# Optimization experiments

Hardware: AMD Instinct MI355X
Metric: run time of the kernel (lower is better)

## Reference

```python
import jax, jax.numpy as jnp
import numpy as np

N_NODES = 100000
N_EDGES = 1600000
D_IN = 128
D_HID = 128
D_OUT = 10
N_GRAPHS = 512


def setup_inputs() -> dict:
    key = jax.random.key(0)
    ks = jax.random.split(key, 12)
    x = jax.random.normal(ks[0], (N_NODES, D_IN), dtype=jnp.float32)
    edge_index = jax.random.randint(ks[1], (2, N_EDGES), 0, N_NODES, dtype=jnp.int64)
    batch = jnp.sort(jax.random.randint(ks[2], (N_NODES,), 0, N_GRAPHS, dtype=jnp.int64))
    s = 1.0 / np.sqrt(D_HID)
    W0 = jax.random.normal(ks[3], (D_HID, D_IN), dtype=jnp.float32) * s
    b0 = jax.random.normal(ks[4], (D_HID,), dtype=jnp.float32) * s
    W1 = jax.random.normal(ks[5], (D_HID, D_HID), dtype=jnp.float32) * s
    b1 = jax.random.normal(ks[6], (D_HID,), dtype=jnp.float32) * s
    W2 = jax.random.normal(ks[7], (D_HID, D_HID), dtype=jnp.float32) * s
    b2 = jax.random.normal(ks[8], (D_HID,), dtype=jnp.float32) * s
    Wg = jax.random.normal(ks[9], (D_OUT, D_HID), dtype=jnp.float32) * s
    bg = jax.random.normal(ks[10], (D_OUT,), dtype=jnp.float32) * s
    return {"x": x, "edge_index": edge_index, "batch": batch,
            "W0": W0, "b0": b0, "W1": W1, "b1": b1, "W2": W2, "b2": b2,
            "Wg": Wg, "bg": bg}


def _gin_conv(x, src, dst, W, b):
    # GINConv with eps=0: Linear(x + sum_{j in N(i)} x_j)
    agg = jax.ops.segment_sum(x[src], dst, num_segments=N_NODES)  # [N, d]
    return (x + agg) @ W.T + b


def reference(x, edge_index, batch, W0, b0, W1, b1, W2, b2, Wg, bg):
    src, dst = edge_index[0], edge_index[1]
    h = jax.nn.relu(_gin_conv(x, src, dst, W0, b0))
    h = jax.nn.relu(_gin_conv(h, src, dst, W1, b1))
    h = _gin_conv(h, src, dst, W2, b2)
    # global_mean_pool over graph ids
    sums = jax.ops.segment_sum(h, batch, num_segments=N_GRAPHS)            # [G, d]
    counts = jax.ops.segment_sum(jnp.ones((N_NODES,), h.dtype), batch, num_segments=N_GRAPHS)
    pooled = sums / jnp.maximum(counts, 1.0)[:, None]                       # [G, d]
    return pooled @ Wg.T + bg                                               # [G, out]
```

## Files before the change

kernel.cpp:

```cpp
#include <hip/hip_runtime.h>

#define N_NODES 100000
#define N_EDGES 1600000
#define N_GRAPHS 512
#define NBUCK 391
#define EPB 8192
#define NB_SCAT ((N_EDGES + EPB - 1) / EPB)
#define CAPB 4864
#define CAP 5120

typedef _Float16 half8 __attribute__((ext_vector_type(8)));
typedef float floatx4 __attribute__((ext_vector_type(4)));

union U16 { uint4 u; half8 h; };

__global__ __launch_bounds__(256) void convert_f16(const float4* __restrict__ X4,
                                                   uint4* __restrict__ Xh) {
    int t = blockIdx.x * 256 + threadIdx.x;
    if (t >= N_NODES * 16) return;
    float4 a = X4[t * 2], b = X4[t * 2 + 1];
    U16 o;
    o.h[0] = (_Float16)a.x; o.h[1] = (_Float16)a.y;
    o.h[2] = (_Float16)a.z; o.h[3] = (_Float16)a.w;
    o.h[4] = (_Float16)b.x; o.h[5] = (_Float16)b.y;
    o.h[6] = (_Float16)b.z; o.h[7] = (_Float16)b.w;
    Xh[t] = o.u;
}

__global__ __launch_bounds__(256) void bucket_scatter(const int* __restrict__ src,
                                                      const int* __restrict__ dst,
                                                      int* __restrict__ gcur,
                                                      unsigned* __restrict__ pairs) {
    __shared__ int cnt[NBUCK];
    __shared__ int base[NBUCK];
    int tid = threadIdx.x;
    for (int i = tid; i < NBUCK; i += 256) cnt[i] = 0;
    __syncthreads();
    int e0 = blockIdx.x * EPB, e1 = min(e0 + EPB, N_EDGES);
    for (int e = e0 + tid; e < e1; e += 256) atomicAdd(&cnt[dst[e] >> 8], 1);
    __syncthreads();
    for (int i = tid; i < NBUCK; i += 256) {
        int v = cnt[i];
        base[i] = i * CAPB + (v ? atomicAdd(&gcur[i], v) : 0);
        cnt[i] = 0;
    }
    __syncthreads();
    for (int e = e0 + tid; e < e1; e += 256) {
        int d = dst[e], b = d >> 8;
        int r = atomicAdd(&cnt[b], 1);
        pairs[base[b] + r] = (unsigned)src[e] | ((unsigned)(d & 255) << 17);
    }
}

__global__ __launch_bounds__(64) void pack_w(const float* __restrict__ W0,
                                             const float* __restrict__ W1,
                                             const float* __restrict__ W2,
                                             uint4* __restrict__ Bp) {
    int b = blockIdx.x;
    int layer = b >> 5;
    int r = b & 31;
    int c = r >> 3, f = r & 7;
    const float* W = (layer == 0) ? W0 : (layer == 1) ? W1 : W2;
    int l = threadIdx.x;
    int col = f * 16 + (l & 15);
    int k0 = c * 32 + (l >> 4) * 8;
    U16 o;
    #pragma unroll
    for (int j = 0; j < 8; ++j) o.h[j] = (_Float16)W[col * 128 + k0 + j];
    Bp[layer * 2048 + (c * 8 + f) * 64 + l] = o.u;
}

__global__ __launch_bounds__(512) void bucket_scan(const int* __restrict__ gcur,
                                                   int* __restrict__ boff,
                                                   int* __restrict__ off) {
    __shared__ int ws[8];
    int tid = threadIdx.x;
    int v = (tid < NBUCK) ? gcur[tid] : 0;
    int lane = tid & 63, w = tid >> 6;
    int incl = v;
    #pragma unroll
    for (int s = 1; s < 64; s <<= 1) { int y = __shfl_up(incl, s, 64); if (lane >= s) incl += y; }
    if (lane == 63) ws[w] = incl;
    __syncthreads();
    if (tid < 8) {
        int t = ws[tid];
        #pragma unroll
        for (int s = 1; s < 8; s <<= 1) { int y = __shfl_up(t, s, 64); if (tid >= s) t += y; }
        ws[tid] = t;
    }
    __syncthreads();
    int excl = (w ? ws[w - 1] : 0) + incl - v;
    if (tid < NBUCK) boff[tid] = excl;
    if (tid == NBUCK - 1) boff[NBUCK] = excl + v;
    if (tid == 0) off[N_NODES] = N_EDGES;
}

__global__ __launch_bounds__(256) void bucket_fine(const unsigned* __restrict__ pairs,
                                                   const int* __restrict__ boff,
                                                   int* __restrict__ off,
                                                   int* __restrict__ srclist) {
    __shared__ int ncnt[256];
    __shared__ int ws[4];
    __shared__ int stage[CAP];
    int tid = threadIdx.x, b = blockIdx.x;
    int eLo = boff[b], m = boff[b + 1] - eLo;
    int sb = b * CAPB;
    ncnt[tid] = 0;
    __syncthreads();
    for (int t = tid; t < m; t += 256) {
        unsigned p = pairs[sb + t];
        atomicAdd(&ncnt[(p >> 17) & 255], 1);
    }
    __syncthreads();
    int v = ncnt[tid];
    int lane = tid & 63, w = tid >> 6;
    int incl = v;
    #pragma unroll
    for (int s = 1; s < 64; s <<= 1) { int y = __shfl_up(incl, s, 64); if (lane >= s) incl += y; }
    if (lane == 63) ws[w] = incl;
    __syncthreads();
    if (tid < 4) {
        int t = ws[tid];
        #pragma unroll
        for (int s = 1; s < 4; s <<= 1) { int y = __shfl_up(t, s, 64); if (tid >= s) t += y; }
        ws[tid] = t;
    }
    __syncthreads();
    int excl = (w ? ws[w - 1] : 0) + incl - v;
    int n = (b << 8) + tid;
    if (n < N_NODES) off[n] = eLo + excl;
    __syncthreads();
    ncnt[tid] = excl;
    __syncthreads();
    for (int t = tid; t < m; t += 256) {
        unsigned p = pairs[sb + t];
        int r = atomicAdd(&ncnt[(p >> 17) & 255], 1);
        int s = (int)(p & 0x1FFFFu);
        if (r < CAP) stage[r] = s;
        else srclist[eLo + r] = s;
    }
    __syncthreads();
    int lim = m < CAP ? m : CAP;
    for (int t = tid; t < lim; t += 256) srclist[eLo + t] = stage[t];
}

__global__ __launch_bounds__(256) void agg_f16(const uint4* __restrict__ Xh,
                                               uint4* __restrict__ Ah,
                                               const int* __restrict__ off,
                                               const int* __restrict__ srclist) {
    int t = blockIdx.x * 256 + threadIdx.x;
    int n = t >> 4, c = t & 15;
    if (n >= N_NODES) return;
    int j0 = off[n], j1 = off[n + 1];
    U16 acc; acc.u = Xh[(size_t)n * 16 + c];
    half8 a = acc.h;
    for (int j = j0; j < j1; j += 8) {
        int idx[8]; unsigned msk[8];
        #pragma unroll
        for (int i = 0; i < 8; ++i) {
            int jj = j + i;
            bool ok = jj < j1;
            int s = srclist[jj];
            idx[i] = ok ? s : n;
            msk[i] = ok ? 0xFFFFFFFFu : 0u;
        }
        U16 v[8];
        #pragma unroll
        for (int i = 0; i < 8; ++i) v[i].u = Xh[(size_t)idx[i] * 16 + c];
        #pragma unroll
        for (int i = 0; i < 8; ++i) {
            v[i].u.x &= msk[i]; v[i].u.y &= msk[i];
            v[i].u.z &= msk[i]; v[i].u.w &= msk[i];
            a += v[i].h;
        }
    }
    U16 o; o.h = a;
    Ah[(size_t)n * 16 + c] = o.u;
}

__global__ __launch_bounds__(256) void gemm_mfma(const _Float16* __restrict__ Ah,
                                                 const uint4* __restrict__ Bp,
                                                 const float* __restrict__ bias,
                                                 _Float16* __restrict__ H, int doRelu) {
    int tid = threadIdx.x;
    int wid = tid >> 6, lane = tid & 63;
    int nbase = blockIdx.x * 128 + wid * 32;
    int lrow = lane & 15;
    int lk = (lane >> 4) * 8;
    int row0 = min(nbase + lrow, N_NODES - 1);
    int row1 = min(nbase + 16 + lrow, N_NODES - 1);

    floatx4 acc[2][8];
    #pragma unroll
    for (int r = 0; r < 2; ++r)
        #pragma unroll
        for (int f = 0; f < 8; ++f) acc[r][f] = (floatx4)0.f;

    #pragma unroll
    for (int c = 0; c < 4; ++c) {
        U16 a0, a1;
        a0.u = *(const uint4*)(Ah + (size_t)row0 * 128 + c * 32 + lk);
        a1.u = *(const uint4*)(Ah + (size_t)row1 * 128 + c * 32 + lk);
        #pragma unroll
        for (int f = 0; f < 8; ++f) {
            U16 b; b.u = Bp[(c * 8 + f) * 64 + lane];
            acc[0][f] = __builtin_amdgcn_mfma_f32_16x16x32_f16(a0.h, b.h, acc[0][f], 0, 0, 0);
            acc[1][f] = __builtin_amdgcn_mfma_f32_16x16x32_f16(a1.h, b.h, acc[1][f], 0, 0, 0);
        }
    }

    int colb = lane & 15;
    int rq = (lane >> 4) * 4;
    #pragma unroll
    for (int f = 0; f < 8; ++f) {
        float bv = bias[f * 16 + colb];
        #pragma unroll
        for (int r = 0; r < 2; ++r) {
            #pragma unroll
            for (int q = 0; q < 4; ++q) {
                int row = nbase + r * 16 + rq + q;
                if (row < N_NODES) {
                    float v = acc[r][f][q] + bv;
                    if (doRelu) v = fmaxf(v, 0.f);
                    H[(size_t)row * 128 + f * 16 + colb] = (_Float16)v;
                }
            }
        }
    }
}

__device__ __forceinline__ int lower_bound_i(const int* a, int n, int val) {
    int lo = 0, hi = n;
    while (lo < hi) {
        int mid = (lo + hi) >> 1;
        if (a[mid] < val) lo = mid + 1; else hi = mid;
    }
    return lo;
}

__global__ __launch_bounds__(256) void pool_kernel(const uint4* __restrict__ Hh,
                                                   const int* __restrict__ batch,
                                                   const float* __restrict__ Wg,
                                                   const float* __restrict__ bg,
                                                   float* __restrict__ out) {
    __shared__ float p[16 * 128];
    __shared__ float pooled[128];
    int g = blockIdx.x, tid = threadIdx.x;
    int c = tid & 15, r = tid >> 4;
    int lo = lower_bound_i(batch, N_NODES, g);
    int hi = lower_bound_i(batch, N_NODES, g + 1);
    float acc[8] = {0, 0, 0, 0, 0, 0, 0, 0};
    for (int i = lo + r; i < hi; i += 16) {
        U16 v; v.u = Hh[(size_t)i * 16 + c];
        #pragma unroll
        for (int k = 0; k < 8; ++k) acc[k] += (float)v.h[k];
    }
    #pragma unroll
    for (int k = 0; k < 8; ++k) p[r * 128 + c * 8 + k] = acc[k];
    __syncthreads();
    if (tid < 128) {
        float s = 0.f;
        #pragma unroll
        for (int q = 0; q < 16; ++q) s += p[q * 128 + tid];
        pooled[tid] = s / fmaxf((float)(hi - lo), 1.0f);
    }
    __syncthreads();
    if (tid < 10) {
        float s = bg[tid];
        #pragma unroll 4
        for (int k = 0; k < 128; ++k) s += pooled[k] * Wg[tid * 128 + k];
        out[g * 10 + tid] = s;
    }
}

extern "C" void kernel_launch(void* const* d_in, const int* in_sizes, int n_in,
                              void* d_out, int out_size, void* d_ws, size_t ws_size,
                              hipStream_t stream) {
    const float* x   = (const float*)d_in[0];
    const int*   ei  = (const int*)d_in[1];
    const int*   bat = (const int*)d_in[2];
    const float* W0  = (const float*)d_in[3];
    const float* b0  = (const float*)d_in[4];
    const float* W1  = (const float*)d_in[5];
    const float* b1  = (const float*)d_in[6];
    const float* W2  = (const float*)d_in[7];
    const float* b2  = (const float*)d_in[8];
    const float* Wg  = (const float*)d_in[9];
    const float* bg  = (const float*)d_in[10];
    float* out = (float*)d_out;

    const int* src = ei;
    const int* dst = ei + N_EDGES;

    char* w = (char*)d_ws;
    _Float16* Ah    = (_Float16*)(w);
    unsigned* pairs = (unsigned*)(w);
    _Float16* P0    = (_Float16*)(w + 25600000);
    _Float16* P1    = (_Float16*)(w + 51200000);
    _Float16* P2    = (_Float16*)(w + 76800000);
    int*    srclist = (int*)(w + 102400000);
    int*    off     = (int*)(w + 108800000);
    uint4*  Bp      = (uint4*)(w + 109300000);
    int*    gcur    = (int*)(w + 109450000);
    int*    boff    = gcur + NBUCK + 1;

    hipMemsetAsync(gcur, 0, NBUCK * sizeof(int), stream);

    bucket_scatter<<<NB_SCAT, 256, 0, stream>>>(src, dst, gcur, pairs);
    bucket_scan<<<1, 512, 0, stream>>>(gcur, boff, off);
    bucket_fine<<<NBUCK, 256, 0, stream>>>(pairs, boff, off, srclist);
    convert_f16<<<(N_NODES * 16 + 255) / 256, 256, 0, stream>>>((const float4*)x, (uint4*)P0);
    pack_w<<<96, 64, 0, stream>>>(W0, W1, W2, Bp);

    int aggGrid  = (N_NODES * 16 + 255) / 256;
    int gemmGrid = (N_NODES + 127) / 128;

    agg_f16<<<aggGrid, 256, 0, stream>>>((const uint4*)P0, (uint4*)Ah, off, srclist);
    gemm_mfma<<<gemmGrid, 256, 0, stream>>>(Ah, Bp, b0, P1, 1);
    agg_f16<<<aggGrid, 256, 0, stream>>>((const uint4*)P1, (uint4*)Ah, off, srclist);
    gemm_mfma<<<gemmGrid, 256, 0, stream>>>(Ah, Bp + 2048, b1, P2, 1);
    agg_f16<<<aggGrid, 256, 0, stream>>>((const uint4*)P2, (uint4*)Ah, off, srclist);
    gemm_mfma<<<gemmGrid, 256, 0, stream>>>(Ah, Bp + 4096, b2, P0, 0);

    pool_kernel<<<N_GRAPHS, 256, 0, stream>>>((const uint4*)P0, bat, Wg, bg, out);
}
```

Baseline: 340.1 us.

## Fold bucket scan into fine pass, merge convert/pack, grid-stride aggregation

Removes the separate single-block bucket_scan kernel by having every bucket_fine block redundantly scan the 391 bucket counts in shared memory. It also merges the feature conversion and weight packing into one launch and makes agg_f16 a grid-stride loop over a fixed 2048 blocks. The goal is fewer kernel launches and less per-launch and tail overhead. In exchange, each fine block now does a small redundant scan, and the persistent aggregation may balance load across blocks less evenly.

```diff
diff --git a/kernel.cpp b/kernel.cpp
--- a/kernel.cpp
+++ b/kernel.cpp
@@ -8,23 +8,45 @@
 #define NB_SCAT ((N_EDGES + EPB - 1) / EPB)
 #define CAPB 4864
 #define CAP 5120
+#define CONV_BLKS 6250
+#define AGG_BLKS 2048
 
 typedef _Float16 half8 __attribute__((ext_vector_type(8)));
 typedef float floatx4 __attribute__((ext_vector_type(4)));
 
 union U16 { uint4 u; half8 h; };
 
-__global__ __launch_bounds__(256) void convert_f16(const float4* __restrict__ X4,
-                                                   uint4* __restrict__ Xh) {
-    int t = blockIdx.x * 256 + threadIdx.x;
-    if (t >= N_NODES * 16) return;
-    float4 a = X4[t * 2], b = X4[t * 2 + 1];
-    U16 o;
-    o.h[0] = (_Float16)a.x; o.h[1] = (_Float16)a.y;
-    o.h[2] = (_Float16)a.z; o.h[3] = (_Float16)a.w;
-    o.h[4] = (_Float16)b.x; o.h[5] = (_Float16)b.y;
-    o.h[6] = (_Float16)b.z; o.h[7] = (_Float16)b.w;
-    Xh[t] = o.u;
+__global__ __launch_bounds__(256) void convert_pack(const float4* __restrict__ X4,
+                                                    uint4* __restrict__ Xh,
+                                                    const float* __restrict__ W0,
+                                                    const float* __restrict__ W1,
+                                                    const float* __restrict__ W2,
+                                                    uint4* __restrict__ Bp) {
+    int bid = blockIdx.x, tid = threadIdx.x;
+    if (bid < CONV_BLKS) {
+        int t = bid * 256 + tid;
+        float4 a = X4[t * 2], b = X4[t * 2 + 1];
+        U16 o;
+        o.h[0] = (_Float16)a.x; o.h[1] = (_Float16)a.y;
+        o.h[2] = (_Float16)a.z; o.h[3] = (_Float16)a.w;
+        o.h[4] = (_Float16)b.x; o.h[5] = (_Float16)b.y;
+        o.h[6] = (_Float16)b.z; o.h[7] = (_Float16)b.w;
+        Xh[t] = o.u;
+    } else {
+        int slice = (bid - CONV_BLKS) * 4 + (tid >> 6);
+        if (slice >= 96) return;
+        int l = tid & 63;
+        int layer = slice >> 5;
+        int r = slice & 31;
+        int c = r >> 3, f = r & 7;
+        const float* W = (layer == 0) ? W0 : (layer == 1) ? W1 : W2;
+        int col = f * 16 + (l & 15);
+        int k0 = c * 32 + (l >> 4) * 8;
+        U16 o;
+        #pragma unroll
+        for (int j = 0; j < 8; ++j) o.h[j] = (_Float16)W[col * 128 + k0 + j];
+        Bp[layer * 2048 + (c * 8 + f) * 64 + l] = o.u;
+    }
 }
 
 __global__ __launch_bounds__(256) void bucket_scatter(const int* __restrict__ src,
@@ -52,68 +74,49 @@
     }
 }
 
-__global__ __launch_bounds__(64) void pack_w(const float* __restrict__ W0,
-                                             const float* __restrict__ W1,
-                                             const float* __restrict__ W2,
-                                             uint4* __restrict__ Bp) {
-    int b = blockIdx.x;
-    int layer = b >> 5;
-    int r = b & 31;
-    int c = r >> 3, f = r & 7;
-    const float* W = (layer == 0) ? W0 : (layer == 1) ? W1 : W2;
-    int l = threadIdx.x;
-    int col = f * 16 + (l & 15);
-    int k0 = c * 32 + (l >> 4) * 8;
-    U16 o;
-    #pragma unroll
-    for (int j = 0; j < 8; ++j) o.h[j] = (_Float16)W[col * 128 + k0 + j];
-    Bp[layer * 2048 + (c * 8 + f) * 64 + l] = o.u;
-}
-
-__global__ __launch_bounds__(512) void bucket_scan(const int* __restrict__ gcur,
-                                                   int* __restrict__ boff,
-                                                   int* __restrict__ off) {
-    __shared__ int ws[8];
-    int tid = threadIdx.x;
-    int v = (tid < NBUCK) ? gcur[tid] : 0;
-    int lane = tid & 63, w = tid >> 6;
-    int incl = v;
-    #pragma unroll
-    for (int s = 1; s < 64; s <<= 1) { int y = __shfl_up(incl, s, 64); if (lane >= s) incl += y; }
-    if (lane == 63) ws[w] = incl;
-    __syncthreads();
-    if (tid < 8) {
-        int t = ws[tid];
-        #pragma unroll
-        for (int s = 1; s < 8; s <<= 1) { int y = __shfl_up(t, s, 64); if (tid >= s) t += y; }
-        ws[tid] = t;
-    }
-    __syncthreads();
-    int excl = (w ? ws[w - 1] : 0) + incl - v;
-    if (tid < NBUCK) boff[tid] = excl;
-    if (tid == NBUCK - 1) boff[NBUCK] = excl + v;
-    if (tid == 0) off[N_NODES] = N_EDGES;
-}
-
 __global__ __launch_bounds__(256) void bucket_fine(const unsigned* __restrict__ pairs,
-                                                   const int* __restrict__ boff,
+                                                   const int* __restrict__ gcur,
                                                    int* __restrict__ off,
                                                    int* __restrict__ srclist) {
+    __shared__ int snap[NBUCK];
     __shared__ int ncnt[256];
     __shared__ int ws[4];
     __shared__ int stage[CAP];
     int tid = threadIdx.x, b = blockIdx.x;
-    int eLo = boff[b], m = boff[b + 1] - eLo;
+    int lane = tid & 63, w = tid >> 6;
+
+    for (int i = tid; i < NBUCK; i += 256) snap[i] = gcur[i];
+    ncnt[tid] = 0;
+    __syncthreads();
+    if (tid < 64) {
+        int carry = 0;
+        for (int base = 0; base < NBUCK; base += 64) {
+            int i = base + tid;
+            int v = (i < NBUCK) ? snap[i] : 0;
+            int incl = v;
+            #pragma unroll
+            for (int s = 1; s < 64; s <<= 1) {
+                int y = __shfl_up(incl, s, 64);
+                if (tid >= s) incl += y;
+            }
+            if (i < NBUCK) snap[i] = carry + incl - v;
+            carry += __shfl(incl, 63, 64);
+        }
+    }
+    __syncthreads();
+    int eLo = snap[b];
+    int eNext = (b == NBUCK - 1) ? N_EDGES : snap[b + 1];
+    int m = eNext - eLo;
     int sb = b * CAPB;
-    ncnt[tid] = 0;
-    __syncthreads();
+    if (b == 0 && tid == 0) off[N_NODES] = N_EDGES;
+    __syncthreads();
+
     for (int t = tid; t < m; t += 256) {
         unsigned p = pairs[sb + t];
         atomicAdd(&ncnt[(p >> 17) & 255], 1);
     }
     __syncthreads();
     int v = ncnt[tid];
-    int lane = tid & 63, w = tid >> 6;
     int incl = v;
     #pragma unroll
     for (int s = 1; s < 64; s <<= 1) { int y = __shfl_up(incl, s, 64); if (lane >= s) incl += y; }
@@ -148,34 +151,36 @@
                                                uint4* __restrict__ Ah,
                                                const int* __restrict__ off,
                                                const int* __restrict__ srclist) {
-    int t = blockIdx.x * 256 + threadIdx.x;
-    int n = t >> 4, c = t & 15;
-    if (n >= N_NODES) return;
-    int j0 = off[n], j1 = off[n + 1];
-    U16 acc; acc.u = Xh[(size_t)n * 16 + c];
-    half8 a = acc.h;
-    for (int j = j0; j < j1; j += 8) {
-        int idx[8]; unsigned msk[8];
-        #pragma unroll
-        for (int i = 0; i < 8; ++i) {
-            int jj = j + i;
-            bool ok = jj < j1;
-            int s = srclist[jj];
-            idx[i] = ok ? s : n;
-            msk[i] = ok ? 0xFFFFFFFFu : 0u;
+    int t0 = blockIdx.x * 256 + threadIdx.x;
+    int c = t0 & 15;
+    const int stride = (AGG_BLKS * 256) >> 4;
+    for (int n = t0 >> 4; n < N_NODES; n += stride) {
+        int j0 = off[n], j1 = off[n + 1];
+        U16 acc; acc.u = Xh[(size_t)n * 16 + c];
+        half8 a = acc.h;
+        for (int j = j0; j < j1; j += 8) {
+            int idx[8]; unsigned msk[8];
+            #pragma unroll
+            for (int i = 0; i < 8; ++i) {
+                int jj = j + i;
+                bool ok = jj < j1;
+                int s = srclist[jj];
+                idx[i] = ok ? s : n;
+                msk[i] = ok ? 0xFFFFFFFFu : 0u;
+            }
+            U16 v[8];
+            #pragma unroll
+            for (int i = 0; i < 8; ++i) v[i].u = Xh[(size_t)idx[i] * 16 + c];
+            #pragma unroll
+            for (int i = 0; i < 8; ++i) {
+                v[i].u.x &= msk[i]; v[i].u.y &= msk[i];
+                v[i].u.z &= msk[i]; v[i].u.w &= msk[i];
+                a += v[i].h;
+            }
         }
-        U16 v[8];
-        #pragma unroll
-        for (int i = 0; i < 8; ++i) v[i].u = Xh[(size_t)idx[i] * 16 + c];
-        #pragma unroll
-        for (int i = 0; i < 8; ++i) {
-            v[i].u.x &= msk[i]; v[i].u.y &= msk[i];
-            v[i].u.z &= msk[i]; v[i].u.w &= msk[i];
-            a += v[i].h;
-        }
-    }
-    U16 o; o.h = a;
-    Ah[(size_t)n * 16 + c] = o.u;
+        U16 o; o.h = a;
+        Ah[(size_t)n * 16 + c] = o.u;
+    }
 }
 
 __global__ __launch_bounds__(256) void gemm_mfma(const _Float16* __restrict__ Ah,
@@ -302,24 +307,21 @@
     int*    off     = (int*)(w + 108800000);
     uint4*  Bp      = (uint4*)(w + 109300000);
     int*    gcur    = (int*)(w + 109450000);
-    int*    boff    = gcur + NBUCK + 1;
 
     hipMemsetAsync(gcur, 0, NBUCK * sizeof(int), stream);
 
     bucket_scatter<<<NB_SCAT, 256, 0, stream>>>(src, dst, gcur, pairs);
-    bucket_scan<<<1, 512, 0, stream>>>(gcur, boff, off);
-    bucket_fine<<<NBUCK, 256, 0, stream>>>(pairs, boff, off, srclist);
-    convert_f16<<<(N_NODES * 16 + 255) / 256, 256, 0, stream>>>((const float4*)x, (uint4*)P0);
-    pack_w<<<96, 64, 0, stream>>>(W0, W1, W2, Bp);
-
-    int aggGrid  = (N_NODES * 16 + 255) / 256;
+    bucket_fine<<<NBUCK, 256, 0, stream>>>(pairs, gcur, off, srclist);
+    convert_pack<<<CONV_BLKS + 24, 256, 0, stream>>>((const float4*)x, (uint4*)P0,
+                                                     W0, W1, W2, Bp);
+
     int gemmGrid = (N_NODES + 127) / 128;
 
-    agg_f16<<<aggGrid, 256, 0, stream>>>((const uint4*)P0, (uint4*)Ah, off, srclist);
+    agg_f16<<<AGG_BLKS, 256, 0, stream>>>((const uint4*)P0, (uint4*)Ah, off, srclist);
     gemm_mfma<<<gemmGrid, 256, 0, stream>>>(Ah, Bp, b0, P1, 1);
-    agg_f16<<<aggGrid, 256, 0, stream>>>((const uint4*)P1, (uint4*)Ah, off, srclist);
+    agg_f16<<<AGG_BLKS, 256, 0, stream>>>((const uint4*)P1, (uint4*)Ah, off, srclist);
     gemm_mfma<<<gemmGrid, 256, 0, stream>>>(Ah, Bp + 2048, b1, P2, 1);
-    agg_f16<<<aggGrid, 256, 0, stream>>>((const uint4*)P2, (uint4*)Ah, off, srclist);
+    agg_f16<<<AGG_BLKS, 256, 0, stream>>>((const uint4*)P2, (uint4*)Ah, off, srclist);
     gemm_mfma<<<gemmGrid, 256, 0, stream>>>(Ah, Bp + 4096, b2, P0, 0);
 
     pool_kernel<<<N_GRAPHS, 256, 0, stream>>>((const uint4*)P0, bat, Wg, bg, out);
```

Measured after the change: 341.9 us. Within noise of the previous version (+0.5%).
